# Performance work log

Hardware: AMD Instinct MI355X
Metric: run time of the kernel (lower is better)

The kernel has to match this reference:

```python
import jax, jax.numpy as jnp
import numpy as np

EPS = 1e-5


def _gc(x, a, w, b):
    # Kipf GCN layer: adj @ (x @ W) + b.  x:[N,din] a:[N,N] w:[din,dout]
    return a @ (x @ w) + b


def _bn(x, gamma, beta):
    # BatchNorm2d(1) in training mode on a [1,1,H,W] tensor: normalize the
    # whole matrix with biased variance.  The surrounding permutes/unsqueezes
    # in the torch code are no-ops for a single-channel full-tensor BN.
    m = jnp.mean(x)
    v = jnp.mean((x - m) ** 2)
    return gamma * (x - m) * jax.lax.rsqrt(v + EPS) + beta


def _block(x, a, w, b, gamma, beta, post_relu):
    h = _bn(jax.nn.relu(_gc(x, a, w, b)), gamma, beta)
    return jax.nn.relu(h) if post_relu else h


def setup_inputs() -> dict:
    key = jax.random.key(0)
    ks = jax.random.split(key, 16)
    N = 8192
    x = jax.random.normal(ks[0], (2, N, 1), dtype=jnp.float32)
    # row-stochastic-ish dense adjacency to keep activations sane
    adj = jax.random.uniform(ks[1], (3, N, N), dtype=jnp.float32) * (2.0 / N)

    def w(k, i, o):
        s = 1.0 / np.sqrt(o)
        return jax.random.uniform(k, (i, o), jnp.float32, -s, s)

    def bvec(k, o):
        s = 1.0 / np.sqrt(o)
        return jax.random.uniform(k, (o,), jnp.float32, -s, s)

    return {
        "x": x, "adj": adj,
        "w11": w(ks[2], 1, 4), "b11": bvec(ks[3], 4),
        "w12": w(ks[4], 4, 1), "b12": bvec(ks[5], 1),
        "w21": w(ks[6], 1, 4), "b21": bvec(ks[7], 4),
        "w22": w(ks[8], 4, 1), "b22": bvec(ks[9], 1),
        "wc1": w(ks[10], 2, 4), "bc1": bvec(ks[11], 4),
        "wc2": w(ks[12], 4, 1), "bc2": bvec(ks[13], 1),
        "gamma": jnp.ones((), jnp.float32),
        "beta": jnp.zeros((), jnp.float32),
    }


def reference(x, adj, w11, b11, w12, b12, w21, b21, w22, b22,
              wc1, bc1, wc2, bc2, gamma, beta):
    F1, F2 = x[0], x[1]          # [N,1]
    A1, A2, A12 = adj[0], adj[1], adj[2]

    F1_1 = _block(F1, A1, w11, b11, gamma, beta, post_relu=False)   # [N,4]
    F1_2 = _block(F1_1, A1, w12, b12, gamma, beta, post_relu=True)  # [N,1]

    F2_1 = _block(F2, A2, w21, b21, gamma, beta, post_relu=False)   # [N,4]
    F2_2 = _block(F2_1, A2, w22, b22, gamma, beta, post_relu=True)  # [N,1]

    F = jnp.concatenate([F1_2, F2_2], axis=1)                       # [N,2]
    F = _block(F, A12, wc1, bc1, gamma, beta, post_relu=False)      # [N,4]
    out = _block(F, A12, wc2, bc2, gamma, beta, post_relu=True)     # [N,1]
    return out
```

## Files before the change

### kernel.cpp

```cpp
#include <hip/hip_runtime.h>

#define N 8192
constexpr float BN_EPS = 1e-5f;

__device__ __forceinline__ void fma4(float4& c, float s, const float4& m) {
    c.x = fmaf(s, m.x, c.x);
    c.y = fmaf(s, m.y, c.y);
    c.z = fmaf(s, m.z, c.z);
    c.w = fmaf(s, m.w, c.w);
}

__device__ __forceinline__ float wave_reduce(float v) {
#pragma unroll
    for (int off = 32; off > 0; off >>= 1) v += __shfl_xor(v, off, 64);
    return v;
}

__device__ __forceinline__ void bn_affine(const float* st, float cnt, float g, float b,
                                          float& alpha, float& delta) {
    float mean = st[0] / cnt;
    float var  = fmaxf(st[1] / cnt - mean * mean, 0.f);
    alpha = g / sqrtf(var + BN_EPS);
    delta = b - alpha * mean;
}

template <int K>
__global__ __launch_bounds__(256) void bigpass(
    const float* __restrict__ A0, const float* __restrict__ M0,
    const float* __restrict__ b0, float* __restrict__ T0, float* __restrict__ st0,
    const float* __restrict__ A1, const float* __restrict__ M1,
    const float* __restrict__ b1, float* __restrict__ T1, float* __restrict__ st1,
    int blocksPerHalf) {
    int bid = blockIdx.x;
    const float* A; const float* M; const float* bv; float* T; float* st;
    if (bid < blocksPerHalf) { A = A0; M = M0; bv = b0; T = T0; st = st0; }
    else { A = A1; M = M1; bv = b1; T = T1; st = st1; bid -= blocksPerHalf; }

    const int lane = threadIdx.x & 63;
    const int wv   = threadIdx.x >> 6;
    const int r0   = (bid * 4 + wv) * 4;

    const float4* Ar0 = (const float4*)(A + (size_t)(r0 + 0) * N);
    const float4* Ar1 = (const float4*)(A + (size_t)(r0 + 1) * N);
    const float4* Ar2 = (const float4*)(A + (size_t)(r0 + 2) * N);
    const float4* Ar3 = (const float4*)(A + (size_t)(r0 + 3) * N);
    const float4* M4  = (const float4*)M;

    if constexpr (K == 4) {
        float4 acc0 = {0, 0, 0, 0}, acc1 = {0, 0, 0, 0};
        float4 acc2 = {0, 0, 0, 0}, acc3 = {0, 0, 0, 0};
        for (int t = lane; t < N / 4; t += 64) {
            float4 m0 = M4[4 * t + 0], m1 = M4[4 * t + 1];
            float4 m2 = M4[4 * t + 2], m3 = M4[4 * t + 3];
            float4 a;
            a = Ar0[t]; fma4(acc0, a.x, m0); fma4(acc0, a.y, m1); fma4(acc0, a.z, m2); fma4(acc0, a.w, m3);
            a = Ar1[t]; fma4(acc1, a.x, m0); fma4(acc1, a.y, m1); fma4(acc1, a.z, m2); fma4(acc1, a.w, m3);
            a = Ar2[t]; fma4(acc2, a.x, m0); fma4(acc2, a.y, m1); fma4(acc2, a.z, m2); fma4(acc2, a.w, m3);
            a = Ar3[t]; fma4(acc3, a.x, m0); fma4(acc3, a.y, m1); fma4(acc3, a.z, m2); fma4(acc3, a.w, m3);
        }
        float r[4][4] = {{acc0.x, acc0.y, acc0.z, acc0.w},
                         {acc1.x, acc1.y, acc1.z, acc1.w},
                         {acc2.x, acc2.y, acc2.z, acc2.w},
                         {acc3.x, acc3.y, acc3.z, acc3.w}};
#pragma unroll
        for (int i = 0; i < 4; i++)
#pragma unroll
            for (int j = 0; j < 4; j++) r[i][j] = wave_reduce(r[i][j]);
        if (lane == 0) {
            float b4[4] = {bv[0], bv[1], bv[2], bv[3]};
            float s = 0.f, ss = 0.f;
#pragma unroll
            for (int i = 0; i < 4; i++) {
                float4 o;
                float* op = (float*)&o;
#pragma unroll
                for (int j = 0; j < 4; j++) {
                    float tv = fmaxf(r[i][j] + b4[j], 0.f);
                    op[j] = tv;
                    s += tv;
                    ss = fmaf(tv, tv, ss);
                }
                ((float4*)T)[r0 + i] = o;
            }
            atomicAdd(&st[0], s);
            atomicAdd(&st[1], ss);
        }
    } else {
        float c0 = 0.f, c1 = 0.f, c2 = 0.f, c3 = 0.f;
        for (int t = lane; t < N / 4; t += 64) {
            float4 m = M4[t];
            float4 a;
            a = Ar0[t]; c0 = fmaf(a.x, m.x, c0); c0 = fmaf(a.y, m.y, c0); c0 = fmaf(a.z, m.z, c0); c0 = fmaf(a.w, m.w, c0);
            a = Ar1[t]; c1 = fmaf(a.x, m.x, c1); c1 = fmaf(a.y, m.y, c1); c1 = fmaf(a.z, m.z, c1); c1 = fmaf(a.w, m.w, c1);
            a = Ar2[t]; c2 = fmaf(a.x, m.x, c2); c2 = fmaf(a.y, m.y, c2); c2 = fmaf(a.z, m.z, c2); c2 = fmaf(a.w, m.w, c2);
            a = Ar3[t]; c3 = fmaf(a.x, m.x, c3); c3 = fmaf(a.y, m.y, c3); c3 = fmaf(a.z, m.z, c3); c3 = fmaf(a.w, m.w, c3);
        }
        c0 = wave_reduce(c0); c1 = wave_reduce(c1);
        c2 = wave_reduce(c2); c3 = wave_reduce(c3);
        if (lane == 0) {
            float bb = bv[0];
            float t0 = fmaxf(c0 + bb, 0.f), t1v = fmaxf(c1 + bb, 0.f);
            float t2v = fmaxf(c2 + bb, 0.f), t3v = fmaxf(c3 + bb, 0.f);
            T[r0 + 0] = t0; T[r0 + 1] = t1v; T[r0 + 2] = t2v; T[r0 + 3] = t3v;
            float s  = t0 + t1v + t2v + t3v;
            float ss = fmaf(t0, t0, fmaf(t1v, t1v, fmaf(t2v, t2v, t3v * t3v)));
            atomicAdd(&st[0], s);
            atomicAdd(&st[1], ss);
        }
    }
}

__global__ void zero_stats(float* stats) {
    if (threadIdx.x < 32) stats[threadIdx.x] = 0.f;
}

__global__ void prep1(const float* __restrict__ x, const float* __restrict__ w11,
                      const float* __restrict__ w21, float* __restrict__ Ma,
                      float* __restrict__ Mb) {
    int i = blockIdx.x * blockDim.x + threadIdx.x;
    if (i >= N) return;
    float x1 = x[i], x2 = x[N + i];
#pragma unroll
    for (int j = 0; j < 4; j++) {
        Ma[i * 4 + j] = x1 * w11[j];
        Mb[i * 4 + j] = x2 * w21[j];
    }
}

__global__ void prep2(const float* __restrict__ stats, const float* __restrict__ gamma,
                      const float* __restrict__ beta, const float* __restrict__ T1,
                      const float* __restrict__ T3, const float* __restrict__ w12,
                      const float* __restrict__ w22, float* __restrict__ M2,
                      float* __restrict__ M4v) {
    int i = blockIdx.x * blockDim.x + threadIdx.x;
    if (i >= N) return;
    float g = *gamma, b = *beta;
    float al0, dl0, al1, dl1;
    bn_affine(stats + 0, (float)(N * 4), g, b, al0, dl0);
    bn_affine(stats + 2, (float)(N * 4), g, b, al1, dl1);
    float4 t1 = ((const float4*)T1)[i];
    float4 t3 = ((const float4*)T3)[i];
    float sw12 = w12[0] + w12[1] + w12[2] + w12[3];
    float sw22 = w22[0] + w22[1] + w22[2] + w22[3];
    M2[i]  = al0 * (t1.x * w12[0] + t1.y * w12[1] + t1.z * w12[2] + t1.w * w12[3]) + dl0 * sw12;
    M4v[i] = al1 * (t3.x * w22[0] + t3.y * w22[1] + t3.z * w22[2] + t3.w * w22[3]) + dl1 * sw22;
}

__global__ void prepc(const float* __restrict__ stats, const float* __restrict__ gamma,
                      const float* __restrict__ beta, const float* __restrict__ T2,
                      const float* __restrict__ T4, const float* __restrict__ wc1,
                      float* __restrict__ Mc) {
    int i = blockIdx.x * blockDim.x + threadIdx.x;
    if (i >= N) return;
    float g = *gamma, b = *beta;
    float al2, dl2, al3, dl3;
    bn_affine(stats + 4, (float)N, g, b, al2, dl2);
    bn_affine(stats + 6, (float)N, g, b, al3, dl3);
    float f1 = fmaxf(al2 * T2[i] + dl2, 0.f);
    float f2 = fmaxf(al3 * T4[i] + dl3, 0.f);
#pragma unroll
    for (int j = 0; j < 4; j++) Mc[i * 4 + j] = f1 * wc1[j] + f2 * wc1[4 + j];
}

__global__ void prepf(const float* __restrict__ stats, const float* __restrict__ gamma,
                      const float* __restrict__ beta, const float* __restrict__ Tc,
                      const float* __restrict__ wc2, float* __restrict__ Mf) {
    int i = blockIdx.x * blockDim.x + threadIdx.x;
    if (i >= N) return;
    float g = *gamma, b = *beta;
    float al4, dl4;
    bn_affine(stats + 8, (float)(N * 4), g, b, al4, dl4);
    float4 tc = ((const float4*)Tc)[i];
    float swc2 = wc2[0] + wc2[1] + wc2[2] + wc2[3];
    Mf[i] = al4 * (tc.x * wc2[0] + tc.y * wc2[1] + tc.z * wc2[2] + tc.w * wc2[3]) + dl4 * swc2;
}

__global__ void finalout(const float* __restrict__ stats, const float* __restrict__ gamma,
                         const float* __restrict__ beta, const float* __restrict__ Tf,
                         float* __restrict__ out) {
    int i = blockIdx.x * blockDim.x + threadIdx.x;
    if (i >= N) return;
    float g = *gamma, b = *beta;
    float al5, dl5;
    bn_affine(stats + 10, (float)N, g, b, al5, dl5);
    out[i] = fmaxf(al5 * Tf[i] + dl5, 0.f);
}

extern "C" void kernel_launch(void* const* d_in, const int* in_sizes, int n_in,
                              void* d_out, int out_size, void* d_ws, size_t ws_size,
                              hipStream_t stream) {
    const float* x     = (const float*)d_in[0];
    const float* adj   = (const float*)d_in[1];
    const float* w11   = (const float*)d_in[2];
    const float* b11   = (const float*)d_in[3];
    const float* w12   = (const float*)d_in[4];
    const float* b12   = (const float*)d_in[5];
    const float* w21   = (const float*)d_in[6];
    const float* b21   = (const float*)d_in[7];
    const float* w22   = (const float*)d_in[8];
    const float* b22   = (const float*)d_in[9];
    const float* wc1   = (const float*)d_in[10];
    const float* bc1   = (const float*)d_in[11];
    const float* wc2   = (const float*)d_in[12];
    const float* bc2   = (const float*)d_in[13];
    const float* gamma = (const float*)d_in[14];
    const float* beta  = (const float*)d_in[15];
    float* out = (float*)d_out;

    const float* A1  = adj;
    const float* A2  = adj + (size_t)N * N;
    const float* A12 = adj + 2 * (size_t)N * N;

    float* wsf   = (float*)d_ws;
    float* stats = wsf;
    float* Ma    = wsf + 32;
    float* Mb    = Ma + N * 4;
    float* T1    = Mb + N * 4;
    float* T3    = T1 + N * 4;
    float* M2    = T3 + N * 4;
    float* M4v   = M2 + N;
    float* T2    = M4v + N;
    float* T4    = T2 + N;
    float* Mc    = T4 + N;
    float* Tc    = Mc + N * 4;
    float* Mf    = Tc + N * 4;
    float* Tf    = Mf + N;

    dim3 blk(256);
    dim3 gsmall((N + 255) / 256);
    const int BPH = N / 16;

    zero_stats<<<1, 32, 0, stream>>>(stats);
    prep1<<<gsmall, blk, 0, stream>>>(x, w11, w21, Ma, Mb);

    bigpass<4><<<dim3(2 * BPH), blk, 0, stream>>>(A1, Ma, b11, T1, stats + 0,
                                                  A2, Mb, b21, T3, stats + 2, BPH);
    prep2<<<gsmall, blk, 0, stream>>>(stats, gamma, beta, T1, T3, w12, w22, M2, M4v);

    bigpass<1><<<dim3(2 * BPH), blk, 0, stream>>>(A1, M2, b12, T2, stats + 4,
                                                  A2, M4v, b22, T4, stats + 6, BPH);
    prepc<<<gsmall, blk, 0, stream>>>(stats, gamma, beta, T2, T4, wc1, Mc);

    bigpass<4><<<dim3(BPH), blk, 0, stream>>>(A12, Mc, bc1, Tc, stats + 8,
                                              A12, Mc, bc1, Tc, stats + 8, BPH);
    prepf<<<gsmall, blk, 0, stream>>>(stats, gamma, beta, Tc, wc2, Mf);

    bigpass<1><<<dim3(BPH), blk, 0, stream>>>(A12, Mf, bc2, Tf, stats + 10,
                                              A12, Mf, bc2, Tf, stats + 10, BPH);
    finalout<<<gsmall, blk, 0, stream>>>(stats, gamma, beta, Tf, out);
}
```

Before: 1.460 ms.

## Transpose M to column-major, stagger column order, reverse second-pass rows, block-reduce stats

Stores the K=4 feature matrices column-major so each wave reads contiguous float4 chunks per feature column, and recomputes the K=4 product as row-by-column dot products. Each wave starts its sweep over the columns at a different chunk, which spreads concurrent reads of M. The K=1 passes now walk rows in reverse block order, so the A rows most recently touched by the previous pass may still be in the large last-level cache. BN statistics are combined per block through shared memory, so only one pair of atomics is issued per block instead of one per wave. The cost is an extra __syncthreads per block and a reliance on cache reuse that is not guaranteed.

```diff
diff --git a/kernel.cpp b/kernel.cpp
--- a/kernel.cpp
+++ b/kernel.cpp
@@ -3,17 +3,18 @@
 #define N 8192
 constexpr float BN_EPS = 1e-5f;
 
-__device__ __forceinline__ void fma4(float4& c, float s, const float4& m) {
-    c.x = fmaf(s, m.x, c.x);
-    c.y = fmaf(s, m.y, c.y);
-    c.z = fmaf(s, m.z, c.z);
-    c.w = fmaf(s, m.w, c.w);
-}
-
 __device__ __forceinline__ float wave_reduce(float v) {
 #pragma unroll
     for (int off = 32; off > 0; off >>= 1) v += __shfl_xor(v, off, 64);
     return v;
+}
+
+__device__ __forceinline__ float dot4acc(float c, const float4 a, const float4 m) {
+    c = fmaf(a.x, m.x, c);
+    c = fmaf(a.y, m.y, c);
+    c = fmaf(a.z, m.z, c);
+    c = fmaf(a.w, m.w, c);
+    return c;
 }
 
 __device__ __forceinline__ void bn_affine(const float* st, float cnt, float g, float b,
@@ -24,7 +25,7 @@
     delta = b - alpha * mean;
 }
 
-template <int K>
+template <int K, int REV>
 __global__ __launch_bounds__(256) void bigpass(
     const float* __restrict__ A0, const float* __restrict__ M0,
     const float* __restrict__ b0, float* __restrict__ T0, float* __restrict__ st0,
@@ -35,78 +36,86 @@
     const float* A; const float* M; const float* bv; float* T; float* st;
     if (bid < blocksPerHalf) { A = A0; M = M0; bv = b0; T = T0; st = st0; }
     else { A = A1; M = M1; bv = b1; T = T1; st = st1; bid -= blocksPerHalf; }
+    if (REV) bid = blocksPerHalf - 1 - bid;
 
     const int lane = threadIdx.x & 63;
     const int wv   = threadIdx.x >> 6;
     const int r0   = (bid * 4 + wv) * 4;
+    const int sgg  = (blockIdx.x * 4 + wv) & 31;
 
     const float4* Ar0 = (const float4*)(A + (size_t)(r0 + 0) * N);
     const float4* Ar1 = (const float4*)(A + (size_t)(r0 + 1) * N);
     const float4* Ar2 = (const float4*)(A + (size_t)(r0 + 2) * N);
     const float4* Ar3 = (const float4*)(A + (size_t)(r0 + 3) * N);
-    const float4* M4  = (const float4*)M;
+
+    __shared__ float sred[2][4];
+    float s_acc = 0.f, ss_acc = 0.f;
 
     if constexpr (K == 4) {
-        float4 acc0 = {0, 0, 0, 0}, acc1 = {0, 0, 0, 0};
-        float4 acc2 = {0, 0, 0, 0}, acc3 = {0, 0, 0, 0};
-        for (int t = lane; t < N / 4; t += 64) {
-            float4 m0 = M4[4 * t + 0], m1 = M4[4 * t + 1];
-            float4 m2 = M4[4 * t + 2], m3 = M4[4 * t + 3];
-            float4 a;
-            a = Ar0[t]; fma4(acc0, a.x, m0); fma4(acc0, a.y, m1); fma4(acc0, a.z, m2); fma4(acc0, a.w, m3);
-            a = Ar1[t]; fma4(acc1, a.x, m0); fma4(acc1, a.y, m1); fma4(acc1, a.z, m2); fma4(acc1, a.w, m3);
-            a = Ar2[t]; fma4(acc2, a.x, m0); fma4(acc2, a.y, m1); fma4(acc2, a.z, m2); fma4(acc2, a.w, m3);
-            a = Ar3[t]; fma4(acc3, a.x, m0); fma4(acc3, a.y, m1); fma4(acc3, a.z, m2); fma4(acc3, a.w, m3);
-        }
-        float r[4][4] = {{acc0.x, acc0.y, acc0.z, acc0.w},
-                         {acc1.x, acc1.y, acc1.z, acc1.w},
-                         {acc2.x, acc2.y, acc2.z, acc2.w},
-                         {acc3.x, acc3.y, acc3.z, acc3.w}};
-#pragma unroll
-        for (int i = 0; i < 4; i++)
-#pragma unroll
-            for (int j = 0; j < 4; j++) r[i][j] = wave_reduce(r[i][j]);
+        const float4* Mt0 = (const float4*)(M + 0 * N);
+        const float4* Mt1 = (const float4*)(M + 1 * N);
+        const float4* Mt2 = (const float4*)(M + 2 * N);
+        const float4* Mt3 = (const float4*)(M + 3 * N);
+        float c[4][4] = {{0.f}};
+        for (int i = 0; i < 32; ++i) {
+            const int t = (((i + sgg) & 31) << 6) + lane;
+            float4 m[4] = {Mt0[t], Mt1[t], Mt2[t], Mt3[t]};
+            float4 a[4] = {Ar0[t], Ar1[t], Ar2[t], Ar3[t]};
+#pragma unroll
+            for (int r = 0; r < 4; r++)
+#pragma unroll
+                for (int j = 0; j < 4; j++) c[r][j] = dot4acc(c[r][j], a[r], m[j]);
+        }
+#pragma unroll
+        for (int r = 0; r < 4; r++)
+#pragma unroll
+            for (int j = 0; j < 4; j++) c[r][j] = wave_reduce(c[r][j]);
         if (lane == 0) {
             float b4[4] = {bv[0], bv[1], bv[2], bv[3]};
-            float s = 0.f, ss = 0.f;
-#pragma unroll
-            for (int i = 0; i < 4; i++) {
+#pragma unroll
+            for (int r = 0; r < 4; r++) {
                 float4 o;
                 float* op = (float*)&o;
 #pragma unroll
                 for (int j = 0; j < 4; j++) {
-                    float tv = fmaxf(r[i][j] + b4[j], 0.f);
+                    float tv = fmaxf(c[r][j] + b4[j], 0.f);
                     op[j] = tv;
-                    s += tv;
-                    ss = fmaf(tv, tv, ss);
+                    s_acc += tv;
+                    ss_acc = fmaf(tv, tv, ss_acc);
                 }
-                ((float4*)T)[r0 + i] = o;
+                ((float4*)T)[r0 + r] = o;
             }
-            atomicAdd(&st[0], s);
-            atomicAdd(&st[1], ss);
         }
     } else {
+        const float4* M4 = (const float4*)M;
         float c0 = 0.f, c1 = 0.f, c2 = 0.f, c3 = 0.f;
-        for (int t = lane; t < N / 4; t += 64) {
+        for (int i = 0; i < 32; ++i) {
+            const int t = (((i + sgg) & 31) << 6) + lane;
             float4 m = M4[t];
-            float4 a;
-            a = Ar0[t]; c0 = fmaf(a.x, m.x, c0); c0 = fmaf(a.y, m.y, c0); c0 = fmaf(a.z, m.z, c0); c0 = fmaf(a.w, m.w, c0);
-            a = Ar1[t]; c1 = fmaf(a.x, m.x, c1); c1 = fmaf(a.y, m.y, c1); c1 = fmaf(a.z, m.z, c1); c1 = fmaf(a.w, m.w, c1);
-            a = Ar2[t]; c2 = fmaf(a.x, m.x, c2); c2 = fmaf(a.y, m.y, c2); c2 = fmaf(a.z, m.z, c2); c2 = fmaf(a.w, m.w, c2);
-            a = Ar3[t]; c3 = fmaf(a.x, m.x, c3); c3 = fmaf(a.y, m.y, c3); c3 = fmaf(a.z, m.z, c3); c3 = fmaf(a.w, m.w, c3);
+            c0 = dot4acc(c0, Ar0[t], m);
+            c1 = dot4acc(c1, Ar1[t], m);
+            c2 = dot4acc(c2, Ar2[t], m);
+            c3 = dot4acc(c3, Ar3[t], m);
         }
         c0 = wave_reduce(c0); c1 = wave_reduce(c1);
         c2 = wave_reduce(c2); c3 = wave_reduce(c3);
         if (lane == 0) {
             float bb = bv[0];
-            float t0 = fmaxf(c0 + bb, 0.f), t1v = fmaxf(c1 + bb, 0.f);
-            float t2v = fmaxf(c2 + bb, 0.f), t3v = fmaxf(c3 + bb, 0.f);
-            T[r0 + 0] = t0; T[r0 + 1] = t1v; T[r0 + 2] = t2v; T[r0 + 3] = t3v;
-            float s  = t0 + t1v + t2v + t3v;
-            float ss = fmaf(t0, t0, fmaf(t1v, t1v, fmaf(t2v, t2v, t3v * t3v)));
-            atomicAdd(&st[0], s);
-            atomicAdd(&st[1], ss);
-        }
+            float t0 = fmaxf(c0 + bb, 0.f), t1 = fmaxf(c1 + bb, 0.f);
+            float t2 = fmaxf(c2 + bb, 0.f), t3 = fmaxf(c3 + bb, 0.f);
+            T[r0 + 0] = t0; T[r0 + 1] = t1; T[r0 + 2] = t2; T[r0 + 3] = t3;
+            s_acc  = t0 + t1 + t2 + t3;
+            ss_acc = fmaf(t0, t0, fmaf(t1, t1, fmaf(t2, t2, t3 * t3)));
+        }
+    }
+
+    if (lane == 0) { sred[0][wv] = s_acc; sred[1][wv] = ss_acc; }
+    __syncthreads();
+    if (threadIdx.x == 0) {
+        float S  = sred[0][0] + sred[0][1] + sred[0][2] + sred[0][3];
+        float SS = sred[1][0] + sred[1][1] + sred[1][2] + sred[1][3];
+        atomicAdd(&st[0], S);
+        atomicAdd(&st[1], SS);
     }
 }
 
@@ -122,8 +131,8 @@
     float x1 = x[i], x2 = x[N + i];
 #pragma unroll
     for (int j = 0; j < 4; j++) {
-        Ma[i * 4 + j] = x1 * w11[j];
-        Mb[i * 4 + j] = x2 * w21[j];
+        Ma[j * N + i] = x1 * w11[j];
+        Mb[j * N + i] = x2 * w21[j];
     }
 }
 
@@ -159,7 +168,7 @@
     float f1 = fmaxf(al2 * T2[i] + dl2, 0.f);
     float f2 = fmaxf(al3 * T4[i] + dl3, 0.f);
 #pragma unroll
-    for (int j = 0; j < 4; j++) Mc[i * 4 + j] = f1 * wc1[j] + f2 * wc1[4 + j];
+    for (int j = 0; j < 4; j++) Mc[j * N + i] = f1 * wc1[j] + f2 * wc1[4 + j];
 }
 
 __global__ void prepf(const float* __restrict__ stats, const float* __restrict__ gamma,
@@ -233,19 +242,19 @@
     zero_stats<<<1, 32, 0, stream>>>(stats);
     prep1<<<gsmall, blk, 0, stream>>>(x, w11, w21, Ma, Mb);
 
-    bigpass<4><<<dim3(2 * BPH), blk, 0, stream>>>(A1, Ma, b11, T1, stats + 0,
-                                                  A2, Mb, b21, T3, stats + 2, BPH);
+    bigpass<4, 0><<<dim3(2 * BPH), blk, 0, stream>>>(A1, Ma, b11, T1, stats + 0,
+                                                     A2, Mb, b21, T3, stats + 2, BPH);
     prep2<<<gsmall, blk, 0, stream>>>(stats, gamma, beta, T1, T3, w12, w22, M2, M4v);
 
-    bigpass<1><<<dim3(2 * BPH), blk, 0, stream>>>(A1, M2, b12, T2, stats + 4,
-                                                  A2, M4v, b22, T4, stats + 6, BPH);
+    bigpass<1, 1><<<dim3(2 * BPH), blk, 0, stream>>>(A1, M2, b12, T2, stats + 4,
+                                                     A2, M4v, b22, T4, stats + 6, BPH);
     prepc<<<gsmall, blk, 0, stream>>>(stats, gamma, beta, T2, T4, wc1, Mc);
 
-    bigpass<4><<<dim3(BPH), blk, 0, stream>>>(A12, Mc, bc1, Tc, stats + 8,
-                                              A12, Mc, bc1, Tc, stats + 8, BPH);
+    bigpass<4, 0><<<dim3(BPH), blk, 0, stream>>>(A12, Mc, bc1, Tc, stats + 8,
+                                                 A12, Mc, bc1, Tc, stats + 8, BPH);
     prepf<<<gsmall, blk, 0, stream>>>(stats, gamma, beta, Tc, wc2, Mf);
 
-    bigpass<1><<<dim3(BPH), blk, 0, stream>>>(A12, Mf, bc2, Tf, stats + 10,
-                                              A12, Mf, bc2, Tf, stats + 10, BPH);
+    bigpass<1, 1><<<dim3(BPH), blk, 0, stream>>>(A12, Mf, bc2, Tf, stats + 10,
+                                                 A12, Mf, bc2, Tf, stats + 10, BPH);
     finalout<<<gsmall, blk, 0, stream>>>(stats, gamma, beta, Tf, out);
 }
```

Result: faster. 1.188 ms (-18.6%).
